# Kernel optimization log

Hardware: AMD Instinct MI355X
Metric: run time of the kernel (lower is better)

The kernel has to match this reference:

```python
import jax, jax.numpy as jnp
import numpy as np

NUM_HEADS = 8
DIM_HEAD_QK = 32
DIM_HEAD_V = 32
BLOCK = 8
HALO = 3
WIN = BLOCK + 2 * HALO  # 14
SCALE = DIM_HEAD_QK ** -0.5


def rel_logits_1d(q, rel_k, permute_mask):
    N, H, W, d = q.shape
    rel_size = rel_k.shape[0]
    win = (rel_size + 1) // 2
    x = jnp.einsum('nhwd,rd->nhwr', q, rel_k)
    x = x.reshape(N * H, W, rel_size)
    x = jnp.pad(x, ((0, 0), (0, 0), (0, 1))).reshape(N * H, -1)
    x = jnp.pad(x, ((0, 0), (0, rel_size - W)))
    x = x.reshape(N * H, W + 1, rel_size)[:, :W, win - 1:]
    x = jnp.broadcast_to(x.reshape(N, H, 1, W, win), (N, H, win, W, win))
    return jnp.transpose(x, permute_mask)


def pos_embed_rel(q, height_rel, width_rel):
    BH, NB, HW, d = q.shape
    qb = q.reshape(-1, BLOCK, BLOCK, d)
    rel_w = rel_logits_1d(qb, width_rel, (0, 1, 3, 2, 4))
    rel_h = rel_logits_1d(jnp.swapaxes(qb, 1, 2), height_rel, (0, 3, 1, 4, 2))
    return (rel_h + rel_w).reshape(BH, NB, HW, WIN * WIN)


def reference(x, q_weight, kv_weight, height_rel, width_rel):
    B, C, H, W = x.shape
    nhb, nwb = H // BLOCK, W // BLOCK
    nb = nhb * nwb
    # 1x1 conv projections
    q = jnp.einsum('bchw,oc->bohw', x, q_weight)
    q = q.reshape(B * NUM_HEADS, DIM_HEAD_QK, nhb, BLOCK, nwb, BLOCK)
    q = jnp.transpose(q, (0, 1, 3, 5, 2, 4)).reshape(B * NUM_HEADS, DIM_HEAD_QK, BLOCK * BLOCK, nb)
    q = jnp.swapaxes(q, 1, 3)  # (BH, nb, BLOCK*BLOCK, dhq)
    kv = jnp.einsum('bchw,oc->bohw', x, kv_weight)
    kv = jnp.pad(kv, ((0, 0), (0, 0), (HALO, HALO), (HALO, HALO)))
    # halo windows: overlapping WINxWIN patches strided by BLOCK
    h_idx = jnp.arange(nhb)[:, None] * BLOCK + jnp.arange(WIN)[None, :]
    w_idx = jnp.arange(nwb)[:, None] * BLOCK + jnp.arange(WIN)[None, :]
    kv = kv[:, :, h_idx, :][:, :, :, :, w_idx]
    kv = jnp.transpose(kv, (0, 1, 2, 4, 3, 5)).reshape(
        B * NUM_HEADS, DIM_HEAD_QK + DIM_HEAD_V, nb, WIN * WIN)
    kv = jnp.transpose(kv, (0, 2, 3, 1))
    k, v = kv[..., :DIM_HEAD_QK], kv[..., DIM_HEAD_QK:]
    attn = jnp.einsum('bnqd,bnkd->bnqk', q, k) * SCALE
    attn = attn + pos_embed_rel(q, height_rel, width_rel)
    attn = jax.nn.softmax(attn, axis=-1)
    out = jnp.einsum('bnqk,bnkd->bnqd', attn, v)
    out = jnp.swapaxes(out, 1, 3)  # (BH, dhv, BLOCK*BLOCK, nb)
    out = out.reshape(-1, BLOCK, BLOCK, nhb, nwb)
    out = jnp.transpose(out, (0, 3, 1, 4, 2)).reshape(B, NUM_HEADS * DIM_HEAD_V, H, W)
    return out


def setup_inputs() -> dict:
    key = jax.random.key(0)
    k1, k2, k3, k4, k5 = jax.random.split(key, 5)
    dim = 256
    std = dim ** -0.5
    x = jax.random.normal(k1, (8, 256, 96, 96), dtype=jnp.float32)
    q_weight = jax.random.normal(k2, (256, 256), dtype=jnp.float32) * std
    kv_weight = jax.random.normal(k3, (512, 256), dtype=jnp.float32) * std
    height_rel = jax.random.normal(k4, (2 * WIN - 1, DIM_HEAD_QK), dtype=jnp.float32) * SCALE
    width_rel = jax.random.normal(k5, (2 * WIN - 1, DIM_HEAD_QK), dtype=jnp.float32) * SCALE
    return {'x': x, 'q_weight': q_weight, 'kv_weight': kv_weight,
            'height_rel': height_rel, 'width_rel': width_rel}
```

## Files before the change

### kernel.cpp

```cpp
#include <hip/hip_runtime.h>
#include <math.h>

#define NPIX 9216
#define SCALE 0.17677669529663687f
#define LOG2E 1.4426950408889634f

typedef __attribute__((ext_vector_type(8))) short bh8;
typedef __attribute__((ext_vector_type(4))) float f4;

__device__ __forceinline__ unsigned short f2bf(float f) {
    unsigned u = __float_as_uint(f);
    u += 0x7fff + ((u >> 16) & 1);
    return (unsigned short)(u >> 16);
}
__device__ __forceinline__ void gload_lds16(const void* g, void* l) {
    __builtin_amdgcn_global_load_lds(
        (const __attribute__((address_space(1))) unsigned int*)g,
        (__attribute__((address_space(3))) unsigned int*)l, 16, 0, 0);
}

__global__ void wconv_kernel(const float* __restrict__ qw, const float* __restrict__ kvw,
                             const float* __restrict__ hrel, const float* __restrict__ wrel,
                             unsigned short* __restrict__ Wb,
                             unsigned short* __restrict__ relb) {
    int bid = blockIdx.x, tid = threadIdx.x;
    if (bid < 768) {
        float v = (bid < 256) ? qw[bid * 256 + tid] : kvw[(bid - 256) * 256 + tid];
        Wb[bid * 256 + tid] = f2bf(v);
    } else {
        int e = (bid - 768) * 256 + tid;
        int half = e >> 10, r = (e >> 5) & 31, d = e & 31;
        float v = 0.0f;
        if (r < 27) v = (half ? wrel : hrel)[r * 32 + d] * LOG2E;
        relb[half * 1024 + r * 32 + d] = f2bf(v);
    }
}

__global__ __launch_bounds__(256) void xtrans_kernel(const float* __restrict__ x,
                                                     unsigned short* __restrict__ xt) {
    int b = blockIdx.z;
    int p0 = blockIdx.x * 128, c0 = blockIdx.y * 128;
    int tid = threadIdx.x;
    __shared__ __align__(16) unsigned short ts[128 * 136];
    const float* xb = x + (size_t)b * 256 * NPIX;
    #pragma unroll
    for (int it = 0; it < 16; ++it) {
        int e = it * 256 + tid;
        int ch = e >> 5, p4 = (e & 31) * 4;
        float4 v = *(const float4*)(xb + (size_t)(c0 + ch) * NPIX + p0 + p4);
        ts[(p4 + 0) * 136 + ch] = f2bf(v.x);
        ts[(p4 + 1) * 136 + ch] = f2bf(v.y);
        ts[(p4 + 2) * 136 + ch] = f2bf(v.z);
        ts[(p4 + 3) * 136 + ch] = f2bf(v.w);
    }
    __syncthreads();
    unsigned short* xtb = xt + (size_t)b * NPIX * 256;
    #pragma unroll
    for (int it = 0; it < 8; ++it) {
        int e = it * 256 + tid;
        int p = e >> 4, ck = (e & 15) * 8;
        *(int4*)(xtb + (size_t)(p0 + p) * 256 + c0 + ck) = *(const int4*)&ts[p * 136 + ck];
    }
}

__global__ __launch_bounds__(256) void proj_kernel(const unsigned short* __restrict__ xt,
                                                   const unsigned short* __restrict__ Wb,
                                                   unsigned short* __restrict__ qb,
                                                   unsigned short* __restrict__ kvb) {
    int flat = blockIdx.x + 72 * (blockIdx.y + 6 * blockIdx.z);
    int w = (flat & 7) * 432 + (flat >> 3);
    int n0 = (w % 6) * 128;
    int m0 = ((w / 6) % 72) * 128;
    int b  = w / 432;
    int tid = threadIdx.x, lane = tid & 63, wave = tid >> 6;
    int ll = lane & 15;
    __shared__ __align__(16) char smem[34816];
    char* As = smem;
    char* Bs = smem + 16384;
    const unsigned short* xtb = xt + (size_t)b * NPIX * 256;

    f4 acc[4][4] = {};
    int wm = (wave & 1) * 64, wn = (wave >> 1) * 64;

    for (int k0 = 0; k0 < 256; k0 += 64) {
        __syncthreads();
        #pragma unroll
        for (int i = 0; i < 4; ++i) {
            int c = wave * 4 + i;
            gload_lds16(xtb + (size_t)(m0 + c * 8 + (lane >> 3)) * 256 + k0 + (lane & 7) * 8,
                        As + c * 1024);
            gload_lds16(Wb + (size_t)(n0 + c * 8 + (lane >> 3)) * 256 + k0 + (lane & 7) * 8,
                        Bs + c * 1024);
        }
        __syncthreads();
        #pragma unroll
        for (int ks = 0; ks < 2; ++ks) {
            bh8 af[4], bf[4];
            #pragma unroll
            for (int i = 0; i < 4; ++i)
                af[i] = *(const bh8*)(As + (wm + i * 16 + ll) * 128 + ks * 64 + (lane >> 4) * 16);
            #pragma unroll
            for (int j = 0; j < 4; ++j)
                bf[j] = *(const bh8*)(Bs + (wn + j * 16 + ll) * 128 + ks * 64 + (lane >> 4) * 16);
            #pragma unroll
            for (int i = 0; i < 4; ++i)
                #pragma unroll
                for (int j = 0; j < 4; ++j)
                    acc[i][j] = __builtin_amdgcn_mfma_f32_16x16x32_bf16(af[i], bf[j], acc[i][j], 0, 0, 0);
        }
    }

    __syncthreads();
    unsigned short* ts = (unsigned short*)smem;
    int q4 = (lane >> 4) * 4;
    #pragma unroll
    for (int i = 0; i < 4; ++i) {
        #pragma unroll
        for (int j = 0; j < 4; ++j) {
            int ch = wn + j * 16 + ll;
            #pragma unroll
            for (int r = 0; r < 4; ++r)
                ts[(wm + i * 16 + q4 + r) * 136 + ch] = f2bf(acc[i][j][r]);
        }
    }
    __syncthreads();
    bool isQ = (n0 < 256);
    #pragma unroll
    for (int it = 0; it < 8; ++it) {
        int e = it * 256 + tid;
        int pixl = e >> 4, ck = (e & 15) * 8;
        int4 v = *(const int4*)&ts[pixl * 136 + ck];
        int pix = m0 + pixl, ch = n0 + ck;
        if (isQ) {
            int head = ch >> 5, d = ch & 31;
            *(int4*)&qb[((size_t)(b * 8 + head) * NPIX + pix) * 32 + d] = v;
        } else {
            int c = ch - 256, head = c >> 6, dv = c & 63;
            *(int4*)&kvb[((size_t)(b * 8 + head) * NPIX + pix) * 64 + dv] = v;
        }
    }
}

__global__ __launch_bounds__(256) void attn_kernel(const unsigned short* __restrict__ qbuf,
                                                   const unsigned short* __restrict__ kvbuf,
                                                   const unsigned short* __restrict__ relb,
                                                   float* __restrict__ out) {
    int flat = blockIdx.x + 144 * blockIdx.y;
    int w = (flat & 7) * 1152 + (flat >> 3);
    int nbid = w % 144, bh = w / 144;
    int b = bh >> 3, head = bh & 7;
    int hb = nbid / 12, wblk = nbid % 12;
    int r0 = hb * 8, c0 = wblk * 8;
    int tid = threadIdx.x, lane = tid & 63, wave = tid >> 6;
    int ll = lane & 15, lq = lane >> 4;
    int m0 = wave * 16;

    __shared__ __align__(16) char smem[50368];
    unsigned short* Vt = (unsigned short*)smem;
    unsigned short* Ks = (unsigned short*)(smem + 15360);
    float*          RhT = (float*)(smem + 33280);
    float*          Rw  = (float*)(smem + 40896);
    unsigned short* Ps  = (unsigned short*)(smem + 15360 + wave * 7424);
    float*          smR = (float*)(smem + 50112);

    const unsigned short* qb  = qbuf  + (size_t)bh * NPIX * 32;
    const unsigned short* kvb = kvbuf + (size_t)bh * NPIX * 64;

    int qp0 = m0 + ll;
    int pixq = (r0 + (qp0 >> 3)) * 96 + c0 + (qp0 & 7);
    bh8 aq = *(const bh8*)&qb[(size_t)pixq * 32 + lq * 8];

    for (int e = tid; e < 896; e += 256) {
        int kp = e >> 2, part = e & 3;
        int a = kp >> 4, b2 = kp & 15;
        int gr = r0 + a - 3, gc = c0 + b2 - 3;
        int4 v = {0, 0, 0, 0};
        if (b2 < 14 && (unsigned)gr < 96u && (unsigned)gc < 96u)
            v = *(const int4*)&kvb[(size_t)(gr * 96 + gc) * 64 + part * 8];
        *(int4*)&Ks[kp * 40 + part * 8] = v;
    }

    #pragma unroll
    for (int it = 0; it < 2; ++it) {
        int e = it * 256 + tid;
        int part = e >> 7, kp2 = e & 127;
        if (kp2 < 112) {
            int a = kp2 >> 3, b2 = (kp2 & 7) * 2;
            int gr = r0 + a - 3, gc = c0 + b2 - 3;
            int4 lo = {0, 0, 0, 0}, hi = {0, 0, 0, 0};
            bool rok = ((kp2 & 7) < 7) && ((unsigned)gr < 96u);
            if (rok && (unsigned)gc < 96u)
                lo = *(const int4*)&kvb[(size_t)(gr * 96 + gc) * 64 + 32 + part * 8];
            if (rok && (unsigned)(gc + 1) < 96u)
                hi = *(const int4*)&kvb[(size_t)(gr * 96 + gc + 1) * 64 + 32 + part * 8];
            int g = kp2 >> 2, kb = b2 & 7;
            const unsigned* lw = (const unsigned*)&lo;
            const unsigned* hw = (const unsigned*)&hi;
            #pragma unroll
            for (int jw = 0; jw < 4; ++jw) {
                unsigned l2 = lw[jw], h2 = hw[jw];
                unsigned v0 = (l2 & 0xffffu) | (h2 << 16);
                unsigned v1 = (l2 >> 16) | (h2 & 0xffff0000u);
                int d0 = part * 8 + jw * 2;
                int s0 = (((jw * 2) & 3) + part) & 3;
                int s1 = (((jw * 2 + 1) & 3) + part) & 3;
                *(unsigned*)&Vt[d0 * 240 + ((g ^ s0) * 8) + kb] = v0;
                *(unsigned*)&Vt[(d0 + 1) * 240 + ((g ^ s1) * 8) + kb] = v1;
            }
        }
    }

    f4 zero4 = {0.f, 0.f, 0.f, 0.f};
    #pragma unroll
    for (int t = 0; t < 2; ++t) {
        int r = t * 16 + ll;
        bh8 hbv = *(const bh8*)&relb[(size_t)r * 32 + lq * 8];
        bh8 wbv = *(const bh8*)&relb[1024 + (size_t)r * 32 + lq * 8];
        f4 ch = __builtin_amdgcn_mfma_f32_16x16x32_bf16(aq, hbv, zero4, 0, 0, 0);
        f4 cw = __builtin_amdgcn_mfma_f32_16x16x32_bf16(aq, wbv, zero4, 0, 0, 0);
        if (r < 28) *(f4*)&RhT[r * 68 + m0 + lq * 4] = ch;
        #pragma unroll
        for (int rr = 0; rr < 4; ++rr)
            Rw[(m0 + lq * 4 + rr) * 36 + r] = cw[rr];
    }

    __syncthreads();

    f4 S[14];
    #pragma unroll
    for (int t = 0; t < 14; ++t) {
        bh8 bk = *(const bh8*)&Ks[(t * 16 + ll) * 40 + lq * 8];
        S[t] = __builtin_amdgcn_mfma_f32_16x16x32_bf16(aq, bk, zero4, 0, 0, 0);
    }

    int row0 = m0 + lq * 4;
    int h = row0 >> 3;
    float nv = (ll < 14) ? 0.0f : -INFINITY;
    float rw4[4];
    #pragma unroll
    for (int rr = 0; rr < 4; ++rr) {
        int row = row0 + rr;
        rw4[rr] = Rw[row * 36 + 13 + ll - (row & 7)] + nv;
    }
    const float SL = SCALE * LOG2E;
    float sm4[4] = {0.f, 0.f, 0.f, 0.f};
    #pragma unroll
    for (int t = 0; t < 14; ++t) {
        f4 rh = *(const f4*)&RhT[(13 + t - h) * 68 + row0];
        #pragma unroll
        for (int rr = 0; rr < 4; ++rr) {
            float lg = S[t][rr] * SL + rh[rr] + rw4[rr];
            float p = __builtin_amdgcn_exp2f(lg);
            S[t][rr] = p;
            sm4[rr] += p;
        }
    }
    #pragma unroll
    for (int rr = 0; rr < 4; ++rr) {
        sm4[rr] += __shfl_xor(sm4[rr], 1);
        sm4[rr] += __shfl_xor(sm4[rr], 2);
        sm4[rr] += __shfl_xor(sm4[rr], 4);
        sm4[rr] += __shfl_xor(sm4[rr], 8);
    }
    if (ll == 0) {
        #pragma unroll
        for (int rr = 0; rr < 4; ++rr) smR[row0 + rr] = sm4[rr];
    }

    __syncthreads();

    #pragma unroll
    for (int t = 0; t < 14; ++t) {
        int col = t * 16 + ll;
        #pragma unroll
        for (int rr = 0; rr < 4; ++rr)
            Ps[(lq * 4 + rr) * 232 + col] = f2bf(S[t][rr]);
    }

    f4 O[2] = {zero4, zero4};
    #pragma unroll
    for (int kt = 0; kt < 7; ++kt) {
        bh8 bp = *(const bh8*)&Ps[ll * 232 + kt * 32 + lq * 8];
        #pragma unroll
        for (int mt = 0; mt < 2; ++mt) {
            int d = mt * 16 + ll;
            int s = ((d & 3) + ((d >> 3) & 3)) & 3;
            bh8 av = *(const bh8*)&Vt[d * 240 + (((kt * 4 + lq) ^ s) * 8)];
            O[mt] = __builtin_amdgcn_mfma_f32_16x16x32_bf16(av, bp, O[mt], 0, 0, 0);
        }
    }

    int qp = m0 + ll;
    float rs = 1.0f / smR[qp];
    int pix = (r0 + (qp >> 3)) * 96 + c0 + (qp & 7);
    float* ob = out + (size_t)(b * 256 + head * 32) * NPIX;
    #pragma unroll
    for (int mt = 0; mt < 2; ++mt) {
        #pragma unroll
        for (int rr = 0; rr < 4; ++rr) {
            int d = mt * 16 + lq * 4 + rr;
            ob[(size_t)d * NPIX + pix] = O[mt][rr] * rs;
        }
    }
}

extern "C" void kernel_launch(void* const* d_in, const int* in_sizes, int n_in,
                              void* d_out, int out_size, void* d_ws, size_t ws_size,
                              hipStream_t stream) {
    const float* x    = (const float*)d_in[0];
    const float* qw   = (const float*)d_in[1];
    const float* kvw  = (const float*)d_in[2];
    const float* hrel = (const float*)d_in[3];
    const float* wrel = (const float*)d_in[4];
    float* out = (float*)d_out;

    char* ws = (char*)d_ws;
    unsigned short* xt    = (unsigned short*)ws;
    unsigned short* Wb    = (unsigned short*)(ws + 37748736);
    unsigned short* relb  = (unsigned short*)(ws + 38141952);
    unsigned short* qbuf  = (unsigned short*)(ws + 38146048);
    unsigned short* kvbuf = (unsigned short*)(ws + 75894784);

    wconv_kernel<<<dim3(776), 256, 0, stream>>>(qw, kvw, hrel, wrel, Wb, relb);
    xtrans_kernel<<<dim3(72, 2, 8), 256, 0, stream>>>(x, xt);
    proj_kernel<<<dim3(72, 6, 8), 256, 0, stream>>>(xt, Wb, qbuf, kvbuf);
    attn_kernel<<<dim3(144, 64), 256, 0, stream>>>(qbuf, kvbuf, relb, out);
}
```

Measured before the change: 273.2 us.

## Load K directly from global into MFMA operands and shrink shared relative-logit tables

Removes the cooperative staging of K into shared memory. Each lane now loads its halo K column straight from global memory into MFMA B operands, with zero-fill for out-of-bounds pixels. The relative-position logit tables become per-wave strips that alias the P buffer, and the block-wide barrier before the QK stage is removed. This cuts LDS traffic and footprint, which may raise occupancy, at the cost of scattered, less coalesced global loads that sit on the QK critical path.

```diff
diff --git a/kernel.cpp b/kernel.cpp
--- a/kernel.cpp
+++ b/kernel.cpp
@@ -155,13 +155,13 @@
     int ll = lane & 15, lq = lane >> 4;
     int m0 = wave * 16;
 
-    __shared__ __align__(16) char smem[50368];
+    __shared__ __align__(16) char smem[45312];
     unsigned short* Vt = (unsigned short*)smem;
-    unsigned short* Ks = (unsigned short*)(smem + 15360);
-    float*          RhT = (float*)(smem + 33280);
-    float*          Rw  = (float*)(smem + 40896);
-    unsigned short* Ps  = (unsigned short*)(smem + 15360 + wave * 7424);
-    float*          smR = (float*)(smem + 50112);
+    char* strip = smem + 15360 + wave * 7424;
+    float*          RhTw = (float*)strip;
+    float*          Rww  = (float*)(strip + 2240);
+    unsigned short* Ps   = (unsigned short*)strip;
+    float*          smR  = (float*)(smem + 45056);
 
     const unsigned short* qb  = qbuf  + (size_t)bh * NPIX * 32;
     const unsigned short* kvb = kvbuf + (size_t)bh * NPIX * 64;
@@ -169,16 +169,6 @@
     int qp0 = m0 + ll;
     int pixq = (r0 + (qp0 >> 3)) * 96 + c0 + (qp0 & 7);
     bh8 aq = *(const bh8*)&qb[(size_t)pixq * 32 + lq * 8];
-
-    for (int e = tid; e < 896; e += 256) {
-        int kp = e >> 2, part = e & 3;
-        int a = kp >> 4, b2 = kp & 15;
-        int gr = r0 + a - 3, gc = c0 + b2 - 3;
-        int4 v = {0, 0, 0, 0};
-        if (b2 < 14 && (unsigned)gr < 96u && (unsigned)gc < 96u)
-            v = *(const int4*)&kvb[(size_t)(gr * 96 + gc) * 64 + part * 8];
-        *(int4*)&Ks[kp * 40 + part * 8] = v;
-    }
 
     #pragma unroll
     for (int it = 0; it < 2; ++it) {
@@ -218,35 +208,41 @@
         bh8 wbv = *(const bh8*)&relb[1024 + (size_t)r * 32 + lq * 8];
         f4 ch = __builtin_amdgcn_mfma_f32_16x16x32_bf16(aq, hbv, zero4, 0, 0, 0);
         f4 cw = __builtin_amdgcn_mfma_f32_16x16x32_bf16(aq, wbv, zero4, 0, 0, 0);
-        if (r < 28) *(f4*)&RhT[r * 68 + m0 + lq * 4] = ch;
-        #pragma unroll
-        for (int rr = 0; rr < 4; ++rr)
-            Rw[(m0 + lq * 4 + rr) * 36 + r] = cw[rr];
-    }
-
-    __syncthreads();
-
+        if (r < 28) *(f4*)&RhTw[r * 20 + lq * 4] = ch;
+        if (r >= 6 && r < 27) {
+            #pragma unroll
+            for (int rr = 0; rr < 4; ++rr)
+                Rww[(lq * 4 + rr) * 23 + (r - 6)] = cw[rr];
+        }
+    }
+
+    int gcq = c0 + ll - 3;
+    bool lane_ok = (ll < 14) && ((unsigned)gcq < 96u);
+    const unsigned short* kcol = kvb + (size_t)gcq * 64 + lq * 8;
     f4 S[14];
     #pragma unroll
     for (int t = 0; t < 14; ++t) {
-        bh8 bk = *(const bh8*)&Ks[(t * 16 + ll) * 40 + lq * 8];
+        int gr = r0 + t - 3;
+        bh8 bk = {};
+        if (lane_ok && (unsigned)gr < 96u)
+            bk = *(const bh8*)(kcol + (size_t)gr * 96 * 64);
         S[t] = __builtin_amdgcn_mfma_f32_16x16x32_bf16(aq, bk, zero4, 0, 0, 0);
     }
 
     int row0 = m0 + lq * 4;
     int h = row0 >> 3;
-    float nv = (ll < 14) ? 0.0f : -INFINITY;
+    bool valid = (ll < 14);
     float rw4[4];
     #pragma unroll
     for (int rr = 0; rr < 4; ++rr) {
         int row = row0 + rr;
-        rw4[rr] = Rw[row * 36 + 13 + ll - (row & 7)] + nv;
+        rw4[rr] = valid ? Rww[(lq * 4 + rr) * 23 + 7 + ll - (row & 7)] : -INFINITY;
     }
     const float SL = SCALE * LOG2E;
     float sm4[4] = {0.f, 0.f, 0.f, 0.f};
     #pragma unroll
     for (int t = 0; t < 14; ++t) {
-        f4 rh = *(const f4*)&RhT[(13 + t - h) * 68 + row0];
+        f4 rh = *(const f4*)&RhTw[(13 + t - h) * 20 + lq * 4];
         #pragma unroll
         for (int rr = 0; rr < 4; ++rr) {
             float lg = S[t][rr] * SL + rh[rr] + rw4[rr];
```

Measured after the change: 301.9 us. 1.1x slower.
